# Kernel tuning notes

Measured on AMD Instinct MI355X. Metric: run time of the kernel, lower is better.

## Reference

```python
import jax, jax.numpy as jnp
import numpy as np
from jax import lax

B, H, N, F = 32, 168, 512, 8
P_STEPS = 24


def setup_inputs() -> dict:
    key = jax.random.key(0)
    ks = jax.random.split(key, 8)
    s = 0.02
    return {
        "x": jax.random.normal(ks[0], (B, H, N, F), dtype=jnp.float32),
        "conv_w": jax.random.normal(ks[1], (N * F, N), dtype=jnp.float32) * s,
        "conv_b": jnp.zeros((N,), dtype=jnp.float32),
        "lstm_k": jax.random.normal(ks[2], (N, 4 * N), dtype=jnp.float32) * s,
        "lstm_rk": jax.random.normal(ks[3], (N, 4 * N), dtype=jnp.float32) * s,
        "lstm_b": jnp.zeros((4 * N,), dtype=jnp.float32),
        "dense_w": jax.random.normal(ks[4], (N, N), dtype=jnp.float32) * s,
        "dense_b": jnp.zeros((N,), dtype=jnp.float32),
        "P": P_STEPS,
    }


def _lstm_cell(h, c, x_t, lstm_k, lstm_rk, lstm_b):
    # Keras LSTMCell gate order: i, f, g(candidate), o
    z = x_t @ lstm_k + h @ lstm_rk + lstm_b  # [B, 4N]
    i, f, g, o = jnp.split(z, 4, axis=-1)
    i = jax.nn.sigmoid(i)
    f = jax.nn.sigmoid(f)
    g = jnp.tanh(g)
    o = jax.nn.sigmoid(o)
    c_new = f * c + i * g
    h_new = o * jnp.tanh(c_new)
    return h_new, c_new


def reference(x, conv_w, conv_b, lstm_k, lstm_rk, lstm_b, dense_w, dense_b, P):
    b, hh, n, f = x.shape
    # Conv1D kernel_size=1 == per-timestep dense projection N*F -> N
    xr = x.reshape(b, hh, n * f) @ conv_w + conv_b  # [B, H, N]

    h0 = jnp.zeros((b, n), dtype=x.dtype)
    c0 = jnp.zeros((b, n), dtype=x.dtype)

    def enc_step(carry, x_t):
        h, c = carry
        h, c = _lstm_cell(h, c, x_t, lstm_k, lstm_rk, lstm_b)
        return (h, c), None

    (h, c), _ = lax.scan(enc_step, (h0, c0), xr.transpose(1, 0, 2))

    def dec_step(carry, _):
        h, c = carry
        h2, c2 = _lstm_cell(h, c, h, lstm_k, lstm_rk, lstm_b)
        return (h2, c2), h2

    _, preds = lax.scan(dec_step, (h, c), None, length=P)  # [P, B, N]
    preds = preds.transpose(1, 0, 2)  # [B, P, N]
    return preds @ dense_w + dense_b
```

## Files before the change

### kernel.cpp

```cpp
#include <hip/hip_runtime.h>
#include <hip/hip_bf16.h>
#include <math.h>

typedef __hip_bfloat16 bf16;
typedef __attribute__((ext_vector_type(8))) short short8;
typedef __attribute__((ext_vector_type(4))) float floatx4;

#define B_  32
#define H_  168
#define N_  512
#define P_  24
#define NF_ 4096
#define G4N 2048
#define M1  (B_*H_)
#define NX  (M1*NF_)
#define TSTEPS (H_+P_)
#define NWG 64
#define HSZ (B_*N_)

__global__ __launch_bounds__(256) void cvt_f32_bf16(const float* __restrict__ in,
                                                    bf16* __restrict__ out, int n4) {
  int i = blockIdx.x * 256 + threadIdx.x;
  if (i < n4) {
    float4 v = ((const float4*)in)[i];
    bf16 o[4] = {__float2bfloat16(v.x), __float2bfloat16(v.y),
                 __float2bfloat16(v.z), __float2bfloat16(v.w)};
    *(ulong1*)(out + (size_t)i * 4) = *(ulong1*)o;
  }
}

__global__ __launch_bounds__(256) void transpose_cvt(const float* __restrict__ in,
                                                     bf16* __restrict__ out,
                                                     int R, int C) {
  __shared__ float t[32][33];
  int bx = blockIdx.x, by = blockIdx.y;
  int tx = threadIdx.x, ty = threadIdx.y;
#pragma unroll
  for (int yy = 0; yy < 32; yy += 8)
    t[ty + yy][tx] = in[(size_t)(by * 32 + ty + yy) * C + bx * 32 + tx];
  __syncthreads();
#pragma unroll
  for (int yy = 0; yy < 32; yy += 8)
    out[(size_t)(bx * 32 + ty + yy) * R + by * 32 + tx] =
        __float2bfloat16(t[tx][ty + yy]);
}

__global__ __launch_bounds__(256) void transpose_krk(const float* __restrict__ k,
                                                     const float* __restrict__ rk,
                                                     bf16* __restrict__ kT,
                                                     bf16* __restrict__ rkT,
                                                     bf16* __restrict__ wcT) {
  __shared__ float t1[32][33], t2[32][33];
  int bx = blockIdx.x, by = blockIdx.y;
  int tx = threadIdx.x, ty = threadIdx.y;
#pragma unroll
  for (int yy = 0; yy < 32; yy += 8) {
    size_t idx = (size_t)(by * 32 + ty + yy) * G4N + bx * 32 + tx;
    t1[ty + yy][tx] = k[idx];
    t2[ty + yy][tx] = rk[idx];
  }
  __syncthreads();
#pragma unroll
  for (int yy = 0; yy < 32; yy += 8) {
    size_t o = (size_t)(bx * 32 + ty + yy) * N_ + by * 32 + tx;
    float a = t1[tx][ty + yy], b = t2[tx][ty + yy];
    kT[o]  = __float2bfloat16(a);
    rkT[o] = __float2bfloat16(b);
    wcT[o] = __float2bfloat16(a + b);
  }
}

template <bool OUT_BF16>
__global__ __launch_bounds__(256) void gemm_bt(const bf16* __restrict__ A,
                                               const bf16* __restrict__ BT,
                                               const float* __restrict__ bias,
                                               void* __restrict__ Cout,
                                               int M, int N, int K, int permute) {
  __shared__ short As[128 * 40];
  __shared__ short Bs[128 * 40];
  int tid  = threadIdx.x;
  int wave = tid >> 6, lane = tid & 63;
  int wm = wave >> 1, wn = wave & 1;
  int quad = lane >> 4, l16 = lane & 15;
  int m0 = blockIdx.y * 128, n0 = blockIdx.x * 128;

  floatx4 acc[4][4];
#pragma unroll
  for (int i = 0; i < 4; i++)
#pragma unroll
    for (int j = 0; j < 4; j++) acc[i][j] = (floatx4){0.f, 0.f, 0.f, 0.f};

  int r0 = tid >> 2;
  int c0 = (tid & 3) * 8;

  for (int k0 = 0; k0 < K; k0 += 32) {
    short8 a0 = *(const short8*)(A  + (size_t)(m0 + r0)      * K + k0 + c0);
    short8 a1 = *(const short8*)(A  + (size_t)(m0 + r0 + 64) * K + k0 + c0);
    short8 b0 = *(const short8*)(BT + (size_t)(n0 + r0)      * K + k0 + c0);
    short8 b1 = *(const short8*)(BT + (size_t)(n0 + r0 + 64) * K + k0 + c0);
    __syncthreads();
    *(short8*)(&As[r0 * 40 + c0])        = a0;
    *(short8*)(&As[(r0 + 64) * 40 + c0]) = a1;
    *(short8*)(&Bs[r0 * 40 + c0])        = b0;
    *(short8*)(&Bs[(r0 + 64) * 40 + c0]) = b1;
    __syncthreads();
    short8 af[4], bfr[4];
#pragma unroll
    for (int i = 0; i < 4; i++)
      af[i] = *(const short8*)(&As[(wm * 64 + i * 16 + l16) * 40 + quad * 8]);
#pragma unroll
    for (int j = 0; j < 4; j++)
      bfr[j] = *(const short8*)(&Bs[(wn * 64 + j * 16 + l16) * 40 + quad * 8]);
#pragma unroll
    for (int i = 0; i < 4; i++)
#pragma unroll
      for (int j = 0; j < 4; j++)
        acc[i][j] = __builtin_amdgcn_mfma_f32_16x16x32_bf16(af[i], bfr[j],
                                                            acc[i][j], 0, 0, 0);
  }
#pragma unroll
  for (int i = 0; i < 4; i++) {
    int row = m0 + wm * 64 + i * 16 + quad * 4;
#pragma unroll
    for (int j = 0; j < 4; j++) {
      int col = n0 + wn * 64 + j * 16 + l16;
      float bv = bias ? bias[col] : 0.f;
#pragma unroll
      for (int r = 0; r < 4; r++) {
        int gr = row + r;
        int orow = permute ? (gr % H_) * B_ + gr / H_ : gr;
        float v = acc[i][j][r] + bv;
        if (OUT_BF16)
          ((bf16*)Cout)[(size_t)orow * N + col] = __float2bfloat16(v);
        else
          ((float*)Cout)[(size_t)orow * N + col] = v;
      }
    }
  }
}

__global__ __launch_bounds__(256) void lstm_persist(
    const bf16* __restrict__ rkT,
    const bf16* __restrict__ wcT,
    const float* __restrict__ bvec,
    const float* __restrict__ xk,
    bf16* __restrict__ hring,
    bf16* __restrict__ preds,
    unsigned* __restrict__ done) {
  __shared__ short Wenc[32][520];
  __shared__ short Wdec[32][520];
  __shared__ float zs[32][33];
  __shared__ bf16  hstage[32][8];

  int tid  = threadIdx.x;
  int bid  = blockIdx.x;
  int wave = tid >> 6, lane = tid & 63;
  int tm = wave >> 1, tn = wave & 1;
  int quad = lane >> 4, l16 = lane & 15;
  int n0 = bid * 8;
  int lc   = tn * 16 + l16;
  int gcol = ((lc >> 3) << 9) + n0 + (lc & 7);
  int brow = tm * 16 + quad * 4;

  for (int idx = tid; idx < 32 * 64; idx += 256) {
    int r = idx >> 6, ck = (idx & 63) << 3;
    int grow = ((r >> 3) << 9) + n0 + (r & 7);
    *(short8*)&Wenc[r][ck] = *(const short8*)(rkT + (size_t)grow * 512 + ck);
    *(short8*)&Wdec[r][ck] = *(const short8*)(wcT + (size_t)grow * 512 + ck);
  }
  float bias_r = bvec[gcol];
  int b = tid >> 3, j = tid & 7;
  int nn = n0 + j;
  float c_reg = 0.f;

  float xkv[4];
  {
    const float* xp = xk + (size_t)brow * G4N + gcol;
#pragma unroll
    for (int r = 0; r < 4; ++r) xkv[r] = xp[(size_t)r * G4N];
  }
  __syncthreads();

  for (int t = 0; t < TSTEPS; ++t) {
    const bf16* h_in  = hring + (size_t)t * HSZ;
    bf16*       h_out = hring + (size_t)(t + 1) * HSZ;
    const short(*Ws)[520] = (t < H_) ? Wenc : Wdec;

    floatx4 acc0 = (floatx4){0.f, 0.f, 0.f, 0.f};
    floatx4 acc1 = (floatx4){0.f, 0.f, 0.f, 0.f};
    const bf16*  ap = h_in + (size_t)(tm * 16 + l16) * 512 + quad * 8;
    const short* bp = &Ws[lc][quad * 8];
#pragma unroll
    for (int k0 = 0; k0 < 512; k0 += 64) {
      short8 av0 = *(const short8*)(ap + k0);
      short8 av1 = *(const short8*)(ap + k0 + 32);
      short8 bv0 = *(const short8*)(bp + k0);
      short8 bv1 = *(const short8*)(bp + k0 + 32);
      acc0 = __builtin_amdgcn_mfma_f32_16x16x32_bf16(av0, bv0, acc0, 0, 0, 0);
      acc1 = __builtin_amdgcn_mfma_f32_16x16x32_bf16(av1, bv1, acc1, 0, 0, 0);
    }
    floatx4 acc = acc0 + acc1;
#pragma unroll
    for (int r = 0; r < 4; ++r)
      zs[brow + r][lc] = acc[r] + bias_r + xkv[r];

    float xn[4] = {0.f, 0.f, 0.f, 0.f};
    if (t + 1 < H_) {
      const float* xp = xk + (size_t)((t + 1) * B_ + brow) * G4N + gcol;
#pragma unroll
      for (int r = 0; r < 4; ++r) xn[r] = xp[(size_t)r * G4N];
    }
    __syncthreads();

    float zi = zs[b][j], zf = zs[b][8 + j], zg = zs[b][16 + j], zo = zs[b][24 + j];
    float ig = 1.f / (1.f + __expf(-zi));
    float fg = 1.f / (1.f + __expf(-zf));
    float gg = tanhf(zg);
    float og = 1.f / (1.f + __expf(-zo));
    c_reg = fg * c_reg + ig * gg;
    float hn = og * tanhf(c_reg);
    hstage[b][j] = __float2bfloat16(hn);
    if (t >= H_)
      preds[(size_t)b * (P_ * N_) + (t - H_) * N_ + nn] = __float2bfloat16(hn);
    __syncthreads();

    if (tid < 64) {
      int bb = tid >> 1, f4 = (tid & 1) * 4;
      unsigned long long v = *(const unsigned long long*)&hstage[bb][f4];
      __hip_atomic_store((unsigned long long*)(h_out + bb * 512 + n0 + f4), v,
                         __ATOMIC_RELAXED, __HIP_MEMORY_SCOPE_AGENT);
    }
    __syncthreads();

    if (tid == 0)
      __hip_atomic_store(&done[(size_t)t * NWG + bid], 1u, __ATOMIC_RELAXED,
                         __HIP_MEMORY_SCOPE_AGENT);
    if (tid < 64) {
      const unsigned* dp = done + (size_t)t * NWG;
      for (;;) {
        unsigned v = __hip_atomic_load(dp + tid, __ATOMIC_RELAXED,
                                       __HIP_MEMORY_SCOPE_AGENT);
        if (__builtin_popcountll(__ballot(v != 0)) == 64) break;
        __builtin_amdgcn_s_sleep(1);
      }
    }
    __builtin_amdgcn_fence(__ATOMIC_ACQUIRE, "workgroup");
    __syncthreads();
#pragma unroll
    for (int r = 0; r < 4; ++r) xkv[r] = xn[r];
  }
}

extern "C" void kernel_launch(void* const* d_in, const int* in_sizes, int n_in,
                              void* d_out, int out_size, void* d_ws, size_t ws_size,
                              hipStream_t stream) {
  const float* x       = (const float*)d_in[0];
  const float* conv_w  = (const float*)d_in[1];
  const float* conv_b  = (const float*)d_in[2];
  const float* lstm_k  = (const float*)d_in[3];
  const float* lstm_rk = (const float*)d_in[4];
  const float* lstm_b  = (const float*)d_in[5];
  const float* dense_w = (const float*)d_in[6];
  const float* dense_b = (const float*)d_in[7];
  float* out = (float*)d_out;

  char* p = (char*)d_ws;
  auto carve = [&](size_t bytes) {
    char* r = p;
    p += (bytes + 255) & ~(size_t)255;
    return r;
  };
  bf16*  xb    = (bf16*)carve((size_t)NX * 2);
  bf16*  xr    = (bf16*)carve((size_t)M1 * N_ * 2);
  float* xk    = (float*)carve((size_t)M1 * G4N * 4);
  bf16*  cwT   = (bf16*)carve((size_t)N_ * NF_ * 2);
  bf16*  kT    = (bf16*)carve((size_t)G4N * N_ * 2);
  bf16*  rkT   = (bf16*)carve((size_t)G4N * N_ * 2);
  bf16*  wcT   = (bf16*)carve((size_t)G4N * N_ * 2);
  bf16*  dwT   = (bf16*)carve((size_t)N_ * N_ * 2);
  bf16*  preds = (bf16*)carve((size_t)B_ * P_ * N_ * 2);
  bf16*  hring = (bf16*)carve((size_t)(TSTEPS + 1) * HSZ * 2);
  unsigned* done = (unsigned*)carve((size_t)TSTEPS * NWG * 4);

  cvt_f32_bf16<<<(NX / 4 + 255) / 256, 256, 0, stream>>>(x, xb, NX / 4);
  dim3 tb(32, 8);
  transpose_cvt<<<dim3(N_ / 32, NF_ / 32), tb, 0, stream>>>(conv_w, cwT, NF_, N_);
  transpose_krk<<<dim3(G4N / 32, N_ / 32), tb, 0, stream>>>(lstm_k, lstm_rk,
                                                            kT, rkT, wcT);
  transpose_cvt<<<dim3(N_ / 32, N_ / 32), tb, 0, stream>>>(dense_w, dwT, N_, N_);
  hipMemsetAsync(hring, 0, (size_t)HSZ * 2, stream);
  hipMemsetAsync(done, 0, (size_t)TSTEPS * NWG * 4, stream);

  gemm_bt<true><<<dim3(N_ / 128, M1 / 128), 256, 0, stream>>>(xb, cwT, conv_b, xr,
                                                              M1, N_, NF_, 1);
  gemm_bt<false><<<dim3(G4N / 128, M1 / 128), 256, 0, stream>>>(xr, kT, nullptr,
                                                                xk, M1, G4N, N_, 0);

  lstm_persist<<<NWG, 256, 0, stream>>>(rkT, wcT, lstm_b, xk, hring, preds, done);

  gemm_bt<false><<<dim3(N_ / 128, (B_ * P_) / 128), 256, 0, stream>>>(
      preds, dwT, dense_b, out, B_ * P_, N_, N_, 0);
}
```

Baseline: 1.130 ms.

## Replace grid barrier with sentinel-polled hidden-state reads in persistent LSTM

```diff
diff --git a/kernel.cpp b/kernel.cpp
--- a/kernel.cpp
+++ b/kernel.cpp
@@ -145,8 +145,7 @@
     const float* __restrict__ bvec,
     const float* __restrict__ xk,
     bf16* __restrict__ hring,
-    bf16* __restrict__ preds,
-    unsigned* __restrict__ done) {
+    bf16* __restrict__ preds) {
   __shared__ short Wenc[32][520];
   __shared__ short Wdec[32][520];
   __shared__ float zs[32][33];
@@ -181,23 +180,49 @@
   }
   __syncthreads();
 
+  const unsigned long long K1 = 0x0001000100010001ULL;
+  const unsigned long long K8 = 0x8000800080010000ULL & 0x8000800080008000ULL;
+  const unsigned long long KH = 0x8000800080008000ULL;
+
   for (int t = 0; t < TSTEPS; ++t) {
     const bf16* h_in  = hring + (size_t)t * HSZ;
     bf16*       h_out = hring + (size_t)(t + 1) * HSZ;
     const short(*Ws)[520] = (t < H_) ? Wenc : Wdec;
 
+    unsigned long long w[32];
+    {
+      const unsigned long long* hp =
+          (const unsigned long long*)(h_in + (size_t)(tm * 16 + l16) * 512) +
+          quad * 2;
+      for (;;) {
+        unsigned long long bad = 0;
+#pragma unroll
+        for (int c = 0; c < 16; ++c) {
+#pragma unroll
+          for (int e = 0; e < 2; ++e) {
+            unsigned long long v = __hip_atomic_load(
+                hp + c * 8 + e, __ATOMIC_RELAXED, __HIP_MEMORY_SCOPE_AGENT);
+            w[c * 2 + e] = v;
+            unsigned long long nv = ~v;
+            bad |= (nv - K1) & v & KH;
+          }
+        }
+        if (__ballot(bad != 0) == 0) break;
+        __builtin_amdgcn_s_sleep(1);
+      }
+    }
+
     floatx4 acc0 = (floatx4){0.f, 0.f, 0.f, 0.f};
     floatx4 acc1 = (floatx4){0.f, 0.f, 0.f, 0.f};
-    const bf16*  ap = h_in + (size_t)(tm * 16 + l16) * 512 + quad * 8;
-    const short* bp = &Ws[lc][quad * 8];
-#pragma unroll
-    for (int k0 = 0; k0 < 512; k0 += 64) {
-      short8 av0 = *(const short8*)(ap + k0);
-      short8 av1 = *(const short8*)(ap + k0 + 32);
-      short8 bv0 = *(const short8*)(bp + k0);
-      short8 bv1 = *(const short8*)(bp + k0 + 32);
-      acc0 = __builtin_amdgcn_mfma_f32_16x16x32_bf16(av0, bv0, acc0, 0, 0, 0);
-      acc1 = __builtin_amdgcn_mfma_f32_16x16x32_bf16(av1, bv1, acc1, 0, 0, 0);
+#pragma unroll
+    for (int c = 0; c < 16; c += 2) {
+      union { unsigned long long u[2]; short8 s; } a0, a1;
+      a0.u[0] = w[c * 2];     a0.u[1] = w[c * 2 + 1];
+      a1.u[0] = w[c * 2 + 2]; a1.u[1] = w[c * 2 + 3];
+      short8 b0 = *(const short8*)&Ws[lc][c * 32 + quad * 8];
+      short8 b1 = *(const short8*)&Ws[lc][(c + 1) * 32 + quad * 8];
+      acc0 = __builtin_amdgcn_mfma_f32_16x16x32_bf16(a0.s, b0, acc0, 0, 0, 0);
+      acc1 = __builtin_amdgcn_mfma_f32_16x16x32_bf16(a1.s, b1, acc1, 0, 0, 0);
     }
     floatx4 acc = acc0 + acc1;
 #pragma unroll
@@ -230,22 +255,6 @@
       __hip_atomic_store((unsigned long long*)(h_out + bb * 512 + n0 + f4), v,
                          __ATOMIC_RELAXED, __HIP_MEMORY_SCOPE_AGENT);
     }
-    __syncthreads();
-
-    if (tid == 0)
-      __hip_atomic_store(&done[(size_t)t * NWG + bid], 1u, __ATOMIC_RELAXED,
-                         __HIP_MEMORY_SCOPE_AGENT);
-    if (tid < 64) {
-      const unsigned* dp = done + (size_t)t * NWG;
-      for (;;) {
-        unsigned v = __hip_atomic_load(dp + tid, __ATOMIC_RELAXED,
-                                       __HIP_MEMORY_SCOPE_AGENT);
-        if (__builtin_popcountll(__ballot(v != 0)) == 64) break;
-        __builtin_amdgcn_s_sleep(1);
-      }
-    }
-    __builtin_amdgcn_fence(__ATOMIC_ACQUIRE, "workgroup");
-    __syncthreads();
 #pragma unroll
     for (int r = 0; r < 4; ++r) xkv[r] = xn[r];
   }
@@ -280,7 +289,6 @@
   bf16*  dwT   = (bf16*)carve((size_t)N_ * N_ * 2);
   bf16*  preds = (bf16*)carve((size_t)B_ * P_ * N_ * 2);
   bf16*  hring = (bf16*)carve((size_t)(TSTEPS + 1) * HSZ * 2);
-  unsigned* done = (unsigned*)carve((size_t)TSTEPS * NWG * 4);
 
   cvt_f32_bf16<<<(NX / 4 + 255) / 256, 256, 0, stream>>>(x, xb, NX / 4);
   dim3 tb(32, 8);
@@ -288,15 +296,15 @@
   transpose_krk<<<dim3(G4N / 32, N_ / 32), tb, 0, stream>>>(lstm_k, lstm_rk,
                                                             kT, rkT, wcT);
   transpose_cvt<<<dim3(N_ / 32, N_ / 32), tb, 0, stream>>>(dense_w, dwT, N_, N_);
+  hipMemsetAsync(hring, 0xFF, (size_t)(TSTEPS + 1) * HSZ * 2, stream);
   hipMemsetAsync(hring, 0, (size_t)HSZ * 2, stream);
-  hipMemsetAsync(done, 0, (size_t)TSTEPS * NWG * 4, stream);
 
   gemm_bt<true><<<dim3(N_ / 128, M1 / 128), 256, 0, stream>>>(xb, cwT, conv_b, xr,
                                                               M1, N_, NF_, 1);
   gemm_bt<false><<<dim3(G4N / 128, M1 / 128), 256, 0, stream>>>(xr, kT, nullptr,
                                                                 xk, M1, G4N, N_, 0);
 
-  lstm_persist<<<NWG, 256, 0, stream>>>(rkT, wcT, lstm_b, xk, hring, preds, done);
+  lstm_persist<<<NWG, 256, 0, stream>>>(rkT, wcT, lstm_b, xk, hring, preds);
 
   gemm_bt<false><<<dim3(N_ / 128, (B_ * P_) / 128), 256, 0, stream>>>(
       preds, dwT, dense_b, out, B_ * P_, N_, N_, 0);
```

New measurement: 1.832 ms. +62.2%, slower.

## Fuse x fp32-to-bf16 conversion into conv GEMM and centralize LSTM barrier

Applied to the files above, without the earlier changes.

```diff
diff --git a/kernel.cpp b/kernel.cpp
--- a/kernel.cpp
+++ b/kernel.cpp
@@ -13,21 +13,9 @@
 #define NF_ 4096
 #define G4N 2048
 #define M1  (B_*H_)
-#define NX  (M1*NF_)
 #define TSTEPS (H_+P_)
 #define NWG 64
 #define HSZ (B_*N_)
-
-__global__ __launch_bounds__(256) void cvt_f32_bf16(const float* __restrict__ in,
-                                                    bf16* __restrict__ out, int n4) {
-  int i = blockIdx.x * 256 + threadIdx.x;
-  if (i < n4) {
-    float4 v = ((const float4*)in)[i];
-    bf16 o[4] = {__float2bfloat16(v.x), __float2bfloat16(v.y),
-                 __float2bfloat16(v.z), __float2bfloat16(v.w)};
-    *(ulong1*)(out + (size_t)i * 4) = *(ulong1*)o;
-  }
-}
 
 __global__ __launch_bounds__(256) void transpose_cvt(const float* __restrict__ in,
                                                      bf16* __restrict__ out,
@@ -139,6 +127,82 @@
   }
 }
 
+__device__ inline short8 cvt8(float4 a, float4 b) {
+  union { bf16 h[8]; short8 s; } u;
+  u.h[0] = __float2bfloat16(a.x); u.h[1] = __float2bfloat16(a.y);
+  u.h[2] = __float2bfloat16(a.z); u.h[3] = __float2bfloat16(a.w);
+  u.h[4] = __float2bfloat16(b.x); u.h[5] = __float2bfloat16(b.y);
+  u.h[6] = __float2bfloat16(b.z); u.h[7] = __float2bfloat16(b.w);
+  return u.s;
+}
+__global__ __launch_bounds__(256) void gemm_a32_bt(const float* __restrict__ A,
+                                                   const bf16* __restrict__ BT,
+                                                   const float* __restrict__ bias,
+                                                   bf16* __restrict__ Cout,
+                                                   int M, int N, int K) {
+  __shared__ short As[128 * 40];
+  __shared__ short Bs[128 * 40];
+  int tid  = threadIdx.x;
+  int wave = tid >> 6, lane = tid & 63;
+  int wm = wave >> 1, wn = wave & 1;
+  int quad = lane >> 4, l16 = lane & 15;
+  int m0 = blockIdx.y * 128, n0 = blockIdx.x * 128;
+
+  floatx4 acc[4][4];
+#pragma unroll
+  for (int i = 0; i < 4; i++)
+#pragma unroll
+    for (int j = 0; j < 4; j++) acc[i][j] = (floatx4){0.f, 0.f, 0.f, 0.f};
+
+  int r0 = tid >> 2;
+  int c0 = (tid & 3) * 8;
+
+  for (int k0 = 0; k0 < K; k0 += 32) {
+    const float* ap0 = A + (size_t)(m0 + r0)      * K + k0 + c0;
+    const float* ap1 = A + (size_t)(m0 + r0 + 64) * K + k0 + c0;
+    float4 fa0 = *(const float4*)ap0, fa1 = *(const float4*)(ap0 + 4);
+    float4 fb0 = *(const float4*)ap1, fb1 = *(const float4*)(ap1 + 4);
+    short8 a0 = cvt8(fa0, fa1);
+    short8 a1 = cvt8(fb0, fb1);
+    short8 b0 = *(const short8*)(BT + (size_t)(n0 + r0)      * K + k0 + c0);
+    short8 b1 = *(const short8*)(BT + (size_t)(n0 + r0 + 64) * K + k0 + c0);
+    __syncthreads();
+    *(short8*)(&As[r0 * 40 + c0])        = a0;
+    *(short8*)(&As[(r0 + 64) * 40 + c0]) = a1;
+    *(short8*)(&Bs[r0 * 40 + c0])        = b0;
+    *(short8*)(&Bs[(r0 + 64) * 40 + c0]) = b1;
+    __syncthreads();
+    short8 af[4], bfr[4];
+#pragma unroll
+    for (int i = 0; i < 4; i++)
+      af[i] = *(const short8*)(&As[(wm * 64 + i * 16 + l16) * 40 + quad * 8]);
+#pragma unroll
+    for (int j = 0; j < 4; j++)
+      bfr[j] = *(const short8*)(&Bs[(wn * 64 + j * 16 + l16) * 40 + quad * 8]);
+#pragma unroll
+    for (int i = 0; i < 4; i++)
+#pragma unroll
+      for (int j = 0; j < 4; j++)
+        acc[i][j] = __builtin_amdgcn_mfma_f32_16x16x32_bf16(af[i], bfr[j],
+                                                            acc[i][j], 0, 0, 0);
+  }
+#pragma unroll
+  for (int i = 0; i < 4; i++) {
+    int row = m0 + wm * 64 + i * 16 + quad * 4;
+#pragma unroll
+    for (int j = 0; j < 4; j++) {
+      int col = n0 + wn * 64 + j * 16 + l16;
+      float bv = bias[col];
+#pragma unroll
+      for (int r = 0; r < 4; r++) {
+        int gr = row + r;
+        int orow = (gr % H_) * B_ + gr / H_;
+        Cout[(size_t)orow * N + col] = __float2bfloat16(acc[i][j][r] + bv);
+      }
+    }
+  }
+}
+
 __global__ __launch_bounds__(256) void lstm_persist(
     const bf16* __restrict__ rkT,
     const bf16* __restrict__ wcT,
@@ -146,7 +210,8 @@
     const float* __restrict__ xk,
     bf16* __restrict__ hring,
     bf16* __restrict__ preds,
-    unsigned* __restrict__ done) {
+    unsigned* __restrict__ done,
+    unsigned* __restrict__ flag) {
   __shared__ short Wenc[32][520];
   __shared__ short Wdec[32][520];
   __shared__ float zs[32][33];
@@ -235,14 +300,23 @@
     if (tid == 0)
       __hip_atomic_store(&done[(size_t)t * NWG + bid], 1u, __ATOMIC_RELAXED,
                          __HIP_MEMORY_SCOPE_AGENT);
-    if (tid < 64) {
-      const unsigned* dp = done + (size_t)t * NWG;
-      for (;;) {
-        unsigned v = __hip_atomic_load(dp + tid, __ATOMIC_RELAXED,
-                                       __HIP_MEMORY_SCOPE_AGENT);
-        if (__builtin_popcountll(__ballot(v != 0)) == 64) break;
+    if (bid == 0) {
+      if (tid < 64) {
+        const unsigned* dp = done + (size_t)t * NWG;
+        for (;;) {
+          unsigned v = __hip_atomic_load(dp + tid, __ATOMIC_RELAXED,
+                                         __HIP_MEMORY_SCOPE_AGENT);
+          if (__builtin_popcountll(__ballot(v != 0)) == 64) break;
+          __builtin_amdgcn_s_sleep(1);
+        }
+        if (tid == 0)
+          __hip_atomic_store(&flag[t], 1u, __ATOMIC_RELAXED,
+                             __HIP_MEMORY_SCOPE_AGENT);
+      }
+    } else if (tid == 0) {
+      while (!__hip_atomic_load(&flag[t], __ATOMIC_RELAXED,
+                                __HIP_MEMORY_SCOPE_AGENT))
         __builtin_amdgcn_s_sleep(1);
-      }
     }
     __builtin_amdgcn_fence(__ATOMIC_ACQUIRE, "workgroup");
     __syncthreads();
@@ -270,7 +344,6 @@
     p += (bytes + 255) & ~(size_t)255;
     return r;
   };
-  bf16*  xb    = (bf16*)carve((size_t)NX * 2);
   bf16*  xr    = (bf16*)carve((size_t)M1 * N_ * 2);
   float* xk    = (float*)carve((size_t)M1 * G4N * 4);
   bf16*  cwT   = (bf16*)carve((size_t)N_ * NF_ * 2);
@@ -281,8 +354,8 @@
   bf16*  preds = (bf16*)carve((size_t)B_ * P_ * N_ * 2);
   bf16*  hring = (bf16*)carve((size_t)(TSTEPS + 1) * HSZ * 2);
   unsigned* done = (unsigned*)carve((size_t)TSTEPS * NWG * 4);
-
-  cvt_f32_bf16<<<(NX / 4 + 255) / 256, 256, 0, stream>>>(x, xb, NX / 4);
+  unsigned* flag = (unsigned*)carve((size_t)TSTEPS * 4);
+
   dim3 tb(32, 8);
   transpose_cvt<<<dim3(N_ / 32, NF_ / 32), tb, 0, stream>>>(conv_w, cwT, NF_, N_);
   transpose_krk<<<dim3(G4N / 32, N_ / 32), tb, 0, stream>>>(lstm_k, lstm_rk,
@@ -290,13 +363,15 @@
   transpose_cvt<<<dim3(N_ / 32, N_ / 32), tb, 0, stream>>>(dense_w, dwT, N_, N_);
   hipMemsetAsync(hring, 0, (size_t)HSZ * 2, stream);
   hipMemsetAsync(done, 0, (size_t)TSTEPS * NWG * 4, stream);
-
-  gemm_bt<true><<<dim3(N_ / 128, M1 / 128), 256, 0, stream>>>(xb, cwT, conv_b, xr,
-                                                              M1, N_, NF_, 1);
+  hipMemsetAsync(flag, 0, (size_t)TSTEPS * 4, stream);
+
+  gemm_a32_bt<<<dim3(N_ / 128, M1 / 128), 256, 0, stream>>>(x, cwT, conv_b, xr,
+                                                            M1, N_, NF_);
   gemm_bt<false><<<dim3(G4N / 128, M1 / 128), 256, 0, stream>>>(xr, kT, nullptr,
                                                                 xk, M1, G4N, N_, 0);
 
-  lstm_persist<<<NWG, 256, 0, stream>>>(rkT, wcT, lstm_b, xk, hring, preds, done);
+  lstm_persist<<<NWG, 256, 0, stream>>>(rkT, wcT, lstm_b, xk, hring, preds,
+                                        done, flag);
 
   gemm_bt<false><<<dim3(N_ / 128, (B_ * P_) / 128), 256, 0, stream>>>(
       preds, dwT, dense_b, out, B_ * P_, N_, N_, 0);
```

Result: no change. 1.117 ms (-1.1%).
